# Optimization experiments

Measured on AMD Instinct MI355X. Metric: run time of the kernel, lower is better.

The kernel has to match this reference:

```python
import jax, jax.numpy as jnp
import numpy as np

B, S, D, H = 2, 2048, 1024, 16
DK = D // H
NEG = -1.0e9


def setup_inputs() -> dict:
    key = jax.random.key(0)
    ks = jax.random.split(key, 11)
    inp = {
        "q": jax.random.normal(ks[0], (B, S, D), jnp.float32),
        "k": jax.random.normal(ks[1], (B, S, D), jnp.float32),
        "v": jax.random.normal(ks[2], (B, S, D), jnp.float32),
        "mask": jnp.tril(jnp.ones((S, S), jnp.int32))[None, None],  # causal [1,1,S,S]
    }
    scale = 0.02
    inp["w_q"] = jax.random.normal(ks[3], (D, D), jnp.float32) * scale
    inp["b_q"] = jnp.zeros((D,), jnp.float32)
    inp["w_k"] = jax.random.normal(ks[4], (D, D), jnp.float32) * scale
    inp["b_k"] = jnp.zeros((D,), jnp.float32)
    inp["w_v"] = jax.random.normal(ks[5], (D, D), jnp.float32) * scale
    inp["b_v"] = jnp.zeros((D,), jnp.float32)
    inp["w_o"] = jax.random.normal(ks[6], (D, D), jnp.float32) * scale
    inp["b_o"] = jnp.zeros((D,), jnp.float32)
    return inp


def reference(q, k, v, mask, w_q, b_q, w_k, b_k, w_v, b_v, w_o, b_o):
    # projections: [B,S,D] -> [B,H,S,DK]
    def proj(x, w, b):
        y = jnp.einsum("bsd,de->bse", x, w) + b
        return y.reshape(B, S, H, DK).transpose(0, 2, 1, 3)

    Q = proj(q, w_q, b_q)
    K = proj(k, w_k, b_k)
    V = proj(v, w_v, b_v)
    # explicit scores matrix, faithful to the original naive attention
    scores = jnp.einsum("bhsd,bhtd->bhst", Q, K) / jnp.sqrt(jnp.float32(DK))
    scores = jnp.where(mask == 0, NEG, scores)
    attn = jax.nn.softmax(scores, axis=-1)  # dropout p=0.0 -> identity
    x = jnp.einsum("bhst,bhtd->bhsd", attn, V)
    x = x.transpose(0, 2, 1, 3).reshape(B, S, D)
    return jnp.einsum("bsd,de->bse", x, w_o) + b_o
```

## Files before the change

### kernel.cpp

```cpp
#include <hip/hip_runtime.h>
#include <hip/hip_bf16.h>

typedef __bf16 bf16;
typedef __bf16 bf16x2 __attribute__((ext_vector_type(2)));
typedef __bf16 bf16x8 __attribute__((ext_vector_type(8)));
typedef float f32x4 __attribute__((ext_vector_type(4)));
typedef float f32x16 __attribute__((ext_vector_type(16)));

#define MFMA16(a, b, c) __builtin_amdgcn_mfma_f32_16x16x32_bf16(a, b, c, 0, 0, 0)
#define MFMA32(a, b, c) __builtin_amdgcn_mfma_f32_32x32x16_bf16(a, b, c, 0, 0, 0)

#define QSCALE 0.18033688f

__global__ __launch_bounds__(256) void convert_k(const float* __restrict__ q,
                                                 const float* __restrict__ k,
                                                 const float* __restrict__ v,
                                                 bf16* __restrict__ qb,
                                                 bf16* __restrict__ kb,
                                                 bf16* __restrict__ vb) {
  const float* src = blockIdx.y == 0 ? q : blockIdx.y == 1 ? k : v;
  bf16* dst = blockIdx.y == 0 ? qb : blockIdx.y == 1 ? kb : vb;
  const size_t i = ((size_t)blockIdx.x * 256 + threadIdx.x) * 8;
  float4 a = *(const float4*)(src + i);
  float4 b = *(const float4*)(src + i + 4);
  bf16x8 o;
  o[0] = (bf16)a.x; o[1] = (bf16)a.y; o[2] = (bf16)a.z; o[3] = (bf16)a.w;
  o[4] = (bf16)b.x; o[5] = (bf16)b.y; o[6] = (bf16)b.z; o[7] = (bf16)b.w;
  *(bf16x8*)(dst + i) = o;
}

__global__ __launch_bounds__(256) void transpose_w(const float* __restrict__ w0,
                                                   const float* __restrict__ w1,
                                                   const float* __restrict__ w2,
                                                   const float* __restrict__ w3,
                                                   bf16* __restrict__ dst) {
  __shared__ bf16 T[64][68];
  const float* W = blockIdx.z == 0 ? w0 : blockIdx.z == 1 ? w1
                   : blockIdx.z == 2 ? w2 : w3;
  bf16* Y = dst + (size_t)blockIdx.z * 1024 * 1024;
  const int t = threadIdx.x, r = t >> 2, c4 = t & 3;
  const int k0 = blockIdx.y * 64, n0 = blockIdx.x * 64;

  const float4* src = (const float4*)(W + (size_t)(k0 + r) * 1024 + n0 + c4 * 16);
  float4 f0 = src[0], f1 = src[1], f2 = src[2], f3 = src[3];
  bf16* row = &T[r][c4 * 16];
  row[0] = (bf16)f0.x; row[1] = (bf16)f0.y; row[2] = (bf16)f0.z; row[3] = (bf16)f0.w;
  row[4] = (bf16)f1.x; row[5] = (bf16)f1.y; row[6] = (bf16)f1.z; row[7] = (bf16)f1.w;
  row[8] = (bf16)f2.x; row[9] = (bf16)f2.y; row[10] = (bf16)f2.z; row[11] = (bf16)f2.w;
  row[12] = (bf16)f3.x; row[13] = (bf16)f3.y; row[14] = (bf16)f3.z; row[15] = (bf16)f3.w;
  __syncthreads();

  bf16x8 o0, o1;
#pragma unroll
  for (int j = 0; j < 8; ++j) o0[j] = T[c4 * 16 + j][r];
#pragma unroll
  for (int j = 0; j < 8; ++j) o1[j] = T[c4 * 16 + 8 + j][r];
  bf16* d = Y + (size_t)(n0 + r) * 1024 + k0 + c4 * 16;
  *(bf16x8*)d = o0;
  *(bf16x8*)(d + 8) = o1;
}

template <int QKV, int MT>
__global__ __launch_bounds__(256, 3) void gemm_p(
    const bf16* __restrict__ xq, const bf16* __restrict__ xk,
    const bf16* __restrict__ xv, const bf16* __restrict__ Wt,
    const float* __restrict__ bq, const float* __restrict__ bk,
    const float* __restrict__ bv, bf16* __restrict__ Qp,
    bf16* __restrict__ Kp, bf16* __restrict__ Vtp, float* __restrict__ Yf) {
  constexpr int AROWS = MT * 32;
  __shared__ bf16 Al[AROWS * 72];
  __shared__ bf16 Bl[128 * 72];

  const int z = QKV ? blockIdx.z : 0;
  const bf16* X = QKV ? (z == 0 ? xq : z == 1 ? xk : xv) : xq;
  const bf16* Bt = Wt + (size_t)z * 1048576;
  const float* bias = QKV ? (z == 0 ? bq : z == 1 ? bk : bv) : bq;
  const float escale = (QKV && z == 0) ? QSCALE : 1.0f;

  const int t = threadIdx.x;
  const int wave = t >> 6, lane = t & 63, quad = lane >> 4, l16 = lane & 15;
  const int wm = (wave >> 1) * (MT * 16), wn = (wave & 1) * 64;
  const int bm = blockIdx.y * AROWS, bn = blockIdx.x * 128;

  constexpr int NA = (MT == 4) ? 4 : 2;
  const int arow = (MT == 4) ? (t >> 1) : (t >> 2);
  const int acol = (MT == 4) ? ((t & 1) * 32) : ((t & 3) * 16);
  const int brow = t >> 1, bcol = (t & 1) * 32;
  const bf16* gA = X + (size_t)(bm + arow) * 1024 + acol;
  const bf16* gB = Bt + (size_t)(bn + brow) * 1024 + bcol;

  bf16x8 ra[NA], rb[4];
#pragma unroll
  for (int j = 0; j < NA; ++j) ra[j] = *(const bf16x8*)(gA + j * 8);
#pragma unroll
  for (int j = 0; j < 4; ++j) rb[j] = *(const bf16x8*)(gB + j * 8);

  f32x4 acc[MT][4] = {};

  for (int kb = 0; kb < 1024; kb += 64) {
    __syncthreads();
#pragma unroll
    for (int j = 0; j < NA; ++j)
      *(bf16x8*)(Al + arow * 72 + acol + j * 8) = ra[j];
#pragma unroll
    for (int j = 0; j < 4; ++j)
      *(bf16x8*)(Bl + brow * 72 + bcol + j * 8) = rb[j];
    __syncthreads();

    if (kb + 64 < 1024) {
#pragma unroll
      for (int j = 0; j < NA; ++j)
        ra[j] = *(const bf16x8*)(gA + kb + 64 + j * 8);
#pragma unroll
      for (int j = 0; j < 4; ++j)
        rb[j] = *(const bf16x8*)(gB + kb + 64 + j * 8);
    }

#pragma unroll
    for (int kk = 0; kk < 2; ++kk) {
      bf16x8 af[MT], bfr[4];
#pragma unroll
      for (int mt = 0; mt < MT; ++mt)
        af[mt] =
            *(const bf16x8*)(Al + (wm + mt * 16 + l16) * 72 + kk * 32 + quad * 8);
#pragma unroll
      for (int nt = 0; nt < 4; ++nt)
        bfr[nt] =
            *(const bf16x8*)(Bl + (wn + nt * 16 + l16) * 72 + kk * 32 + quad * 8);
#pragma unroll
      for (int mt = 0; mt < MT; ++mt)
#pragma unroll
        for (int nt = 0; nt < 4; ++nt)
          acc[mt][nt] = MFMA16(af[mt], bfr[nt], acc[mt][nt]);
    }
  }

  if (QKV && z == 2) {
    bf16* Tt = Al;
    const int b = bm >> 11;
    __syncthreads();
#pragma unroll
    for (int half = 0; half < 2; ++half) {
      if ((wave & 1) == half) {
#pragma unroll
        for (int nt = 0; nt < 4; ++nt) {
          const int ln = nt * 16 + l16;
          const float bia = bias[bn + half * 64 + ln];
#pragma unroll
          for (int mt = 0; mt < 4; ++mt)
#pragma unroll
            for (int r = 0; r < 4; ++r) {
              const int m = wm + mt * 16 + quad * 4 + r;
              Tt[ln * 136 + m] = (bf16)(acc[mt][nt][r] + bia);
            }
        }
      }
      __syncthreads();
      {
        const int ln = t >> 2, seg = (t & 3) * 32;
        const int gn = bn + half * 64 + ln;
        const int h = gn >> 6, dk = gn & 63;
        const int s0 = (bm & 2047) + seg;
        bf16* dstp = Vtp + ((size_t)(b * 16 + h) * 64 + dk) * 2048 + s0;
        const bf16* srcp = Tt + ln * 136 + seg;
#pragma unroll
        for (int j = 0; j < 4; ++j)
          *(bf16x8*)(dstp + j * 8) = *(const bf16x8*)(srcp + j * 8);
      }
      __syncthreads();
    }
  } else {
#pragma unroll
    for (int mt = 0; mt < MT; ++mt)
#pragma unroll
      for (int nt = 0; nt < 4; ++nt) {
        const int gn = bn + wn + nt * 16 + l16;
        const float bia = bias[gn];
#pragma unroll
        for (int r = 0; r < 4; ++r) {
          const int gm = bm + wm + mt * 16 + quad * 4 + r;
          const float val = (acc[mt][nt][r] + bia) * escale;
          if (!QKV) {
            Yf[(size_t)gm * 1024 + gn] = val;
          } else {
            const int b = gm >> 11, s = gm & 2047;
            const int h = gn >> 6, dk = gn & 63;
            bf16* Y = (z == 0) ? Qp : Kp;
            Y[((size_t)(b * 16 + h) * 2048 + s) * 64 + dk] = (bf16)val;
          }
        }
      }
  }
}

__global__ __launch_bounds__(256, 2) void attn_k(const bf16* __restrict__ Q,
                                                 const bf16* __restrict__ K,
                                                 const bf16* __restrict__ Vt,
                                                 bf16* __restrict__ X) {
  __shared__ __align__(16) char LB[65536];
  __shared__ float Ex[2048];
  __shared__ float ExR[128];
  __shared__ float rsL[4][32];

  bf16* KB = (bf16*)LB;
  bf16* VB = (bf16*)(LB + 32768);

  const int t = threadIdx.x;
  const int wave = t >> 6, lane = t & 63;
  const int cl = lane & 31, h = lane >> 5;
  const int qsub = wave & 1, kpart = wave >> 1;

  const int n = blockIdx.x;
  const int xcd = n & 7, mm = n >> 3;
  const int bh = xcd + 8 * (mm & 3);
  const int pairx = mm >> 2;
  const int b = bh >> 4, hh = bh & 15;

  const bf16* Qb = Q + (size_t)bh * 2048 * 64;
  const bf16* Kb = K + (size_t)bh * 2048 * 64;
  const bf16* Vb = Vt + (size_t)bh * 64 * 2048;

  const int sr = t >> 2, sc4 = t & 3;
  const int swz = (sr & 7) << 4;
  const int d0 = sr * 128 + ((sc4 * 32) ^ swz);
  const int d1 = sr * 128 + ((sc4 * 32 + 16) ^ swz);
  const int fswz = (cl & 7) << 4;

  for (int ph = 0; ph < 2; ++ph) {
    const int qt = ph ? 31 - pairx : pairx;
    const int ntiles = qt + 1;
    const int S = (ntiles + 1) >> 1;
    const int q0 = qt * 64 + qsub * 32;

    bf16x8 qf[4];
#pragma unroll
    for (int ks = 0; ks < 4; ++ks)
      qf[ks] = *(const bf16x8*)(Qb + (size_t)(q0 + cl) * 64 + ks * 16 + h * 8);

    f32x16 o0 = {}, o1 = {};
    float rs = 0.f;

#pragma unroll
    for (int p = 0; p < 2; ++p) {
      const bf16* gk = Kb + (size_t)(p * 64 + sr) * 64 + sc4 * 16;
      const bf16* gv = Vb + (size_t)sr * 2048 + p * 64 + sc4 * 16;
      bf16x8 ka = *(const bf16x8*)gk, kb2 = *(const bf16x8*)(gk + 8);
      bf16x8 va = *(const bf16x8*)gv, vb2 = *(const bf16x8*)(gv + 8);
      char* Kd = (char*)(KB + p * 4096);
      char* Vd = (char*)(VB + p * 4096);
      *(bf16x8*)(Kd + d0) = ka;  *(bf16x8*)(Kd + d1) = kb2;
      *(bf16x8*)(Vd + d0) = va;  *(bf16x8*)(Vd + d1) = vb2;
    }
    __syncthreads();

    for (int ss = 0; ss < S; ++ss) {
      const int par = ss & 1;
      const bool more = (ss + 1) < S;
      bf16x8 rk[2][2], rv[2][2];
      if (more) {
#pragma unroll
        for (int p = 0; p < 2; ++p) {
          const int kt2 = 2 * (ss + 1) + p;
          const bf16* gk = Kb + (size_t)kt2 * 4096 + sr * 64 + sc4 * 16;
          const bf16* gv = Vb + (size_t)sr * 2048 + kt2 * 64 + sc4 * 16;
          rk[p][0] = *(const bf16x8*)gk;
          rk[p][1] = *(const bf16x8*)(gk + 8);
          rv[p][0] = *(const bf16x8*)gv;
          rv[p][1] = *(const bf16x8*)(gv + 8);
        }
      }

      const int kt = 2 * ss + kpart;
      if (kt < ntiles) {
        const int k0 = kt * 64;
        const char* Kc = (const char*)(KB + (par * 2 + kpart) * 4096);
        const char* Vc = (const char*)(VB + (par * 2 + kpart) * 4096);
        const bool interior = (k0 + 63) <= q0;

        f32x16 s0v = {}, s1v = {};
#pragma unroll
        for (int ks = 0; ks < 4; ++ks) {
          const int cb = ks * 32 + h * 16;
          bf16x8 f0 = *(const bf16x8*)(Kc + cl * 128 + (cb ^ fswz));
          bf16x8 f1 = *(const bf16x8*)(Kc + (cl + 32) * 128 + (cb ^ fswz));
          s0v = MFMA32(f0, qf[ks], s0v);
          s1v = MFMA32(f1, qf[ks], s1v);
        }

        unsigned pk[8][2];
        float ts = 0.f;
        auto smax = [&](const f32x16& sv, int mk) {
#pragma unroll
          for (int sl = 0; sl < 4; ++sl)
#pragma unroll
            for (int p = 0; p < 2; ++p) {
              float e0 = exp2f(sv[sl * 4 + 2 * p]);
              float e1 = exp2f(sv[sl * 4 + 2 * p + 1]);
              if (!interior) {
                const int ky = k0 + mk * 32 + 8 * sl + 4 * h + 2 * p;
                const int qg = q0 + cl;
                if (ky > qg) e0 = 0.f;
                if (ky + 1 > qg) e1 = 0.f;
              }
              ts += e0 + e1;
              union { bf16x2 v; unsigned u; } cv;
              cv.v[0] = (bf16)e0;
              cv.v[1] = (bf16)e1;
              pk[mk * 4 + sl][p] = cv.u;
            }
        };
        smax(s0v, 0);
        smax(s1v, 1);
        rs += ts;

        bf16x8 pf[4];
#pragma unroll
        for (int ks = 0; ks < 4; ++ks) {
          const unsigned oe0 = pk[2 * ks][0], oe1 = pk[2 * ks][1];
          const unsigned oo0 = pk[2 * ks + 1][0], oo1 = pk[2 * ks + 1][1];
          const unsigned pe0 = (unsigned)__shfl_xor((int)oe0, 32, 64);
          const unsigned pe1 = (unsigned)__shfl_xor((int)oe1, 32, 64);
          const unsigned po0 = (unsigned)__shfl_xor((int)oo0, 32, 64);
          const unsigned po1 = (unsigned)__shfl_xor((int)oo1, 32, 64);
          union { unsigned u[4]; bf16x8 v; } fu;
          fu.u[0] = h ? po0 : oe0;
          fu.u[1] = h ? po1 : oe1;
          fu.u[2] = h ? oo0 : pe0;
          fu.u[3] = h ? oo1 : pe1;
          pf[ks] = fu.v;
        }

#pragma unroll
        for (int ks = 0; ks < 4; ++ks) {
          const int cb = ks * 32 + h * 16;
          bf16x8 v0f = *(const bf16x8*)(Vc + cl * 128 + (cb ^ fswz));
          bf16x8 v1f = *(const bf16x8*)(Vc + (cl + 32) * 128 + (cb ^ fswz));
          o0 = MFMA32(pf[ks], v0f, o0);
          o1 = MFMA32(pf[ks], v1f, o1);
        }
      }

      if (more) {
#pragma unroll
        for (int p = 0; p < 2; ++p) {
          char* Kd = (char*)(KB + ((par ^ 1) * 2 + p) * 4096);
          char* Vd = (char*)(VB + ((par ^ 1) * 2 + p) * 4096);
          *(bf16x8*)(Kd + d0) = rk[p][0];
          *(bf16x8*)(Kd + d1) = rk[p][1];
          *(bf16x8*)(Vd + d0) = rv[p][0];
          *(bf16x8*)(Vd + d1) = rv[p][1];
        }
      }
      __syncthreads();
    }

    if (kpart == 0) {
      float* e = Ex + qsub * 1024;
#pragma unroll
      for (int i = 0; i < 16; ++i) e[i * 64 + lane] = o0[i];
      ExR[qsub * 64 + lane] = rs;
    }
    __syncthreads();
    if (kpart == 1) {
      const float* e = Ex + qsub * 1024;
#pragma unroll
      for (int i = 0; i < 16; ++i) o0[i] += e[i * 64 + lane];
      rs += ExR[qsub * 64 + lane];
    }
    __syncthreads();
    if (kpart == 0) {
      float* e = Ex + qsub * 1024;
#pragma unroll
      for (int i = 0; i < 16; ++i) e[i * 64 + lane] = o1[i];
    }
    __syncthreads();
    if (kpart == 1) {
      const float* e = Ex + qsub * 1024;
#pragma unroll
      for (int i = 0; i < 16; ++i) o1[i] += e[i * 64 + lane];

      const float rtot = rs + __shfl_xor(rs, 32, 64);
      rsL[wave][cl] = 1.0f / rtot;
      __builtin_amdgcn_s_waitcnt(0xC07F);
      bf16* Xb = X + (size_t)b * 2048 * 1024 + hh * 64;
#pragma unroll
      for (int g = 0; g < 16; ++g) {
        const int qr = (g & 3) + 8 * (g >> 2) + 4 * h;
        const float ri = rsL[wave][qr];
        const int qg = q0 + qr;
        Xb[(size_t)qg * 1024 + cl] = (bf16)(o0[g] * ri);
        Xb[(size_t)qg * 1024 + 32 + cl] = (bf16)(o1[g] * ri);
      }
    }
    __syncthreads();
  }
}

extern "C" void kernel_launch(void* const* d_in, const int* in_sizes, int n_in,
                              void* d_out, int out_size, void* d_ws,
                              size_t ws_size, hipStream_t stream) {
  const float* q = (const float*)d_in[0];
  const float* k = (const float*)d_in[1];
  const float* v = (const float*)d_in[2];
  const float* w_q = (const float*)d_in[4];
  const float* b_q = (const float*)d_in[5];
  const float* w_k = (const float*)d_in[6];
  const float* b_k = (const float*)d_in[7];
  const float* w_v = (const float*)d_in[8];
  const float* b_v = (const float*)d_in[9];
  const float* w_o = (const float*)d_in[10];
  const float* b_o = (const float*)d_in[11];

  bf16* ws = (bf16*)d_ws;
  const size_t NELEM = (size_t)4096 * 1024;
  bf16* Qp = ws;
  bf16* Kp = ws + NELEM;
  bf16* Vtp = ws + 2 * NELEM;
  bf16* Xp = ws + 3 * NELEM;
  bf16* Wt = ws + 4 * NELEM;
  bf16* Wto = Wt + 3145728;
  bf16* qb = Xp;
  bf16* kb = (bf16*)d_out;
  bf16* vb = kb + NELEM;

  convert_k<<<dim3(2048, 3), 256, 0, stream>>>(q, k, v, qb, kb, vb);
  transpose_w<<<dim3(16, 16, 4), 256, 0, stream>>>(w_q, w_k, w_v, w_o, Wt);

  gemm_p<1, 4><<<dim3(8, 32, 3), 256, 0, stream>>>(
      qb, kb, vb, Wt, b_q, b_k, b_v, Qp, Kp, Vtp, nullptr);
  attn_k<<<dim3(512), 256, 0, stream>>>(Qp, Kp, Vtp, Xp);
  gemm_p<0, 2><<<dim3(8, 64), 256, 0, stream>>>(
      Xp, nullptr, nullptr, Wto, b_o, nullptr, nullptr, nullptr, nullptr,
      nullptr, (float*)d_out);
}
```

Before: 231.7 us.

## Load GEMM tiles directly into LDS with XOR-swizzled layout

The projection GEMM used to stage its A and B tiles through registers with a one-step prefetch, then write them into padded shared memory (72-element stride). It now uses `global_load_lds` to copy 16-byte chunks straight from global memory into an unpadded 64-element-stride LDS tile. Bank conflicts are avoided with an XOR swizzle on the 16-byte chunk index. This removes the VGPR staging and the explicit LDS stores, but loads are no longer prefetched one iteration ahead, so memory latency is only hidden by other resident blocks.

```diff
diff --git a/kernel.cpp b/kernel.cpp
--- a/kernel.cpp
+++ b/kernel.cpp
@@ -11,6 +11,12 @@
 #define MFMA32(a, b, c) __builtin_amdgcn_mfma_f32_32x32x16_bf16(a, b, c, 0, 0, 0)
 
 #define QSCALE 0.18033688f
+
+__device__ __forceinline__ void gld16(const bf16* g, bf16* l) {
+  __builtin_amdgcn_global_load_lds(
+      (const __attribute__((address_space(1))) void*)g,
+      (__attribute__((address_space(3))) void*)l, 16, 0, 0);
+}
 
 __global__ __launch_bounds__(256) void convert_k(const float* __restrict__ q,
                                                  const float* __restrict__ k,
@@ -68,8 +74,9 @@
     const float* __restrict__ bv, bf16* __restrict__ Qp,
     bf16* __restrict__ Kp, bf16* __restrict__ Vtp, float* __restrict__ Yf) {
   constexpr int AROWS = MT * 32;
-  __shared__ bf16 Al[AROWS * 72];
-  __shared__ bf16 Bl[128 * 72];
+  __shared__ __align__(16) bf16 SH[AROWS * 64 + 128 * 64];
+  bf16* Al = SH;
+  bf16* Bl = SH + AROWS * 64;
 
   const int z = QKV ? blockIdx.z : 0;
   const bf16* X = QKV ? (z == 0 ? xq : z == 1 ? xk : xv) : xq;
@@ -82,51 +89,48 @@
   const int wm = (wave >> 1) * (MT * 16), wn = (wave & 1) * 64;
   const int bm = blockIdx.y * AROWS, bn = blockIdx.x * 128;
 
-  constexpr int NA = (MT == 4) ? 4 : 2;
-  const int arow = (MT == 4) ? (t >> 1) : (t >> 2);
-  const int acol = (MT == 4) ? ((t & 1) * 32) : ((t & 3) * 16);
-  const int brow = t >> 1, bcol = (t & 1) * 32;
-  const bf16* gA = X + (size_t)(bm + arow) * 1024 + acol;
-  const bf16* gB = Bt + (size_t)(bn + brow) * 1024 + bcol;
-
-  bf16x8 ra[NA], rb[4];
-#pragma unroll
-  for (int j = 0; j < NA; ++j) ra[j] = *(const bf16x8*)(gA + j * 8);
-#pragma unroll
-  for (int j = 0; j < 4; ++j) rb[j] = *(const bf16x8*)(gB + j * 8);
+  const int lr = (lane >> 3) & 7, lc = lane & 7;
+  constexpr int NAC = AROWS / 32;
+  const bf16* gA[NAC];
+  bf16* lA[NAC];
+#pragma unroll
+  for (int i = 0; i < NAC; ++i) {
+    const int q = wave * NAC + i;
+    gA[i] = X + (size_t)(bm + 8 * q + lr) * 1024 + 8 * (lc ^ lr);
+    lA[i] = Al + q * 512;
+  }
+  const bf16* gB[4];
+  bf16* lB[4];
+#pragma unroll
+  for (int i = 0; i < 4; ++i) {
+    const int q = wave * 4 + i;
+    gB[i] = Bt + (size_t)(bn + 8 * q + lr) * 1024 + 8 * (lc ^ lr);
+    lB[i] = Bl + q * 512;
+  }
 
   f32x4 acc[MT][4] = {};
+  const int fswz = (l16 & 7) << 4;
 
   for (int kb = 0; kb < 1024; kb += 64) {
     __syncthreads();
 #pragma unroll
-    for (int j = 0; j < NA; ++j)
-      *(bf16x8*)(Al + arow * 72 + acol + j * 8) = ra[j];
-#pragma unroll
-    for (int j = 0; j < 4; ++j)
-      *(bf16x8*)(Bl + brow * 72 + bcol + j * 8) = rb[j];
-    __syncthreads();
-
-    if (kb + 64 < 1024) {
-#pragma unroll
-      for (int j = 0; j < NA; ++j)
-        ra[j] = *(const bf16x8*)(gA + kb + 64 + j * 8);
-#pragma unroll
-      for (int j = 0; j < 4; ++j)
-        rb[j] = *(const bf16x8*)(gB + kb + 64 + j * 8);
-    }
+    for (int i = 0; i < NAC; ++i) gld16(gA[i] + kb, lA[i]);
+#pragma unroll
+    for (int i = 0; i < 4; ++i) gld16(gB[i] + kb, lB[i]);
+    __syncthreads();
 
 #pragma unroll
     for (int kk = 0; kk < 2; ++kk) {
+      const int cb = (kk * 64 + quad * 16) ^ fswz;
       bf16x8 af[MT], bfr[4];
 #pragma unroll
       for (int mt = 0; mt < MT; ++mt)
-        af[mt] =
-            *(const bf16x8*)(Al + (wm + mt * 16 + l16) * 72 + kk * 32 + quad * 8);
+        af[mt] = *(const bf16x8*)((const char*)Al +
+                                  (wm + mt * 16 + l16) * 128 + cb);
 #pragma unroll
       for (int nt = 0; nt < 4; ++nt)
-        bfr[nt] =
-            *(const bf16x8*)(Bl + (wn + nt * 16 + l16) * 72 + kk * 32 + quad * 8);
+        bfr[nt] = *(const bf16x8*)((const char*)Bl +
+                                   (wn + nt * 16 + l16) * 128 + cb);
 #pragma unroll
       for (int mt = 0; mt < MT; ++mt)
 #pragma unroll
@@ -136,7 +140,7 @@
   }
 
   if (QKV && z == 2) {
-    bf16* Tt = Al;
+    bf16* Tt = SH;
     const int b = bm >> 11;
     __syncthreads();
 #pragma unroll
```

Measured after the change: 227.8 us. No clear change (-1.7%).
